# Kernel tuning notes

Hardware: AMD Instinct MI355X
Metric: run time of the kernel (lower is better)

## Reference

```python
import jax, jax.numpy as jnp
import numpy as np
import math

D_MODEL, N_HEADS, D_FF = 1024, 16, 4096
B, S = 2, 2048
EPS = 1e-8
NEG = -1e9


def setup_inputs() -> dict:
    key = jax.random.key(0)
    ks = jax.random.split(key, 8)
    sc = 0.02
    return {
        "x": jax.random.normal(ks[0], (B, S, D_MODEL), dtype=jnp.float32),
        "mask": jnp.ones((B, 1, 1, S), dtype=jnp.int32),
        "Wq": jax.random.normal(ks[1], (D_MODEL, D_MODEL), dtype=jnp.float32) * sc,
        "bq": jnp.zeros((D_MODEL,), dtype=jnp.float32),
        "Wk": jax.random.normal(ks[2], (D_MODEL, D_MODEL), dtype=jnp.float32) * sc,
        "bk": jnp.zeros((D_MODEL,), dtype=jnp.float32),
        "Wv": jax.random.normal(ks[3], (D_MODEL, D_MODEL), dtype=jnp.float32) * sc,
        "bv": jnp.zeros((D_MODEL,), dtype=jnp.float32),
        "Wo": jax.random.normal(ks[4], (D_MODEL, D_MODEL), dtype=jnp.float32) * sc,
        "bo": jnp.zeros((D_MODEL,), dtype=jnp.float32),
        "W1": jax.random.normal(ks[5], (D_FF, D_MODEL), dtype=jnp.float32) * sc,
        "b1": jnp.zeros((D_FF,), dtype=jnp.float32),
        "W2": jax.random.normal(ks[6], (D_MODEL, D_FF), dtype=jnp.float32) * sc,
        "b2": jnp.zeros((D_MODEL,), dtype=jnp.float32),
        "g1": jnp.ones((1, 1, 1), dtype=jnp.float32),
        "be1": jnp.zeros((1, 1, 1), dtype=jnp.float32),
        "g2": jnp.ones((1, 1, 1), dtype=jnp.float32),
        "be2": jnp.zeros((1, 1, 1), dtype=jnp.float32),
    }


def _layernorm(x, gamma, beta):
    # Matches torch: mean / unbiased std (ddof=1), eps added to std (not var)
    mean = jnp.mean(x, axis=-1, keepdims=True)
    std = jnp.std(x, axis=-1, keepdims=True, ddof=1)
    return gamma * (x - mean) / (std + EPS) + beta


def reference(x, mask, Wq, bq, Wk, bk, Wv, bv, Wo, bo, W1, b1, W2, b2, g1, be1, g2, be2):
    dk = D_MODEL // N_HEADS

    # --- pre-norm self-attention + residual ---
    h = _layernorm(x, g1, be1)
    q = h @ Wq.T + bq
    k = h @ Wk.T + bk
    v = h @ Wv.T + bv
    # [B,S,D] -> [B,H,S,dk]
    q = q.reshape(B, S, N_HEADS, dk).transpose(0, 2, 1, 3)
    k = k.reshape(B, S, N_HEADS, dk).transpose(0, 2, 1, 3)
    v = v.reshape(B, S, N_HEADS, dk).transpose(0, 2, 1, 3)
    scores = jnp.einsum('bhqd,bhkd->bhqk', q, k) / math.sqrt(dk)
    scores = jnp.where(mask == 0, NEG, scores)
    attn = jax.nn.softmax(scores, axis=-1)
    ctx = jnp.einsum('bhqk,bhkd->bhqd', attn, v)  # [B,H,S,dk]
    ctx = ctx.transpose(0, 2, 1, 3).reshape(B, S, D_MODEL)
    x = x + (ctx @ Wo.T + bo)

    # --- pre-norm FFN + residual ---
    h2 = _layernorm(x, g2, be2)
    f = jax.nn.relu(h2 @ W1.T + b1) @ W2.T + b2
    return x + f
```

## Files before the change

kernel.cpp:

```cpp
#include <hip/hip_runtime.h>
#include <math.h>

#define D_MODEL 1024
#define N_HEADS 16
#define DK      64
#define D_FF    4096
#define BB      2
#define SS      2048
#define ROWS    (BB * SS)
#define EPS     1e-8f
#define NEG     -1e9f
#define QSCALE  0.1803368801111f
#define DEFER_THR 11.541560327f

union F4 { float4 v; float f[4]; };

typedef __attribute__((ext_vector_type(8))) short   bf16x8;
typedef __attribute__((ext_vector_type(4))) float   f32x4;

__device__ __forceinline__ unsigned short f2bf(float f) {
    union { float f; unsigned u; } a; a.f = f;
    unsigned r = a.u + 0x7FFFu + ((a.u >> 16) & 1u);
    return (unsigned short)(r >> 16);
}

__device__ __forceinline__ float exp2_fast(float x) {
    float r;
    asm("v_exp_f32 %0, %1" : "=v"(r) : "v"(x));
    return r;
}

__device__ __forceinline__ unsigned cvt_pk_bf16(float lo, float hi) {
    unsigned r;
    asm("v_cvt_pk_bf16_f32 %0, %1, %2" : "=v"(r) : "v"(lo), "v"(hi));
    return r;
}

__device__ __forceinline__ void gload16(const void* g, void* l) {
    __builtin_amdgcn_global_load_lds(
        (const __attribute__((address_space(1))) unsigned int*)g,
        (__attribute__((address_space(3))) unsigned int*)l, 16, 0, 0);
}

__global__ __launch_bounds__(256) void ln_bf16_kernel(const float* __restrict__ x,
                                                      const float* __restrict__ g,
                                                      const float* __restrict__ be,
                                                      unsigned short* __restrict__ out) {
    __shared__ float sm[8];
    const int row = blockIdx.x;
    float4 v = ((const float4*)(x + (size_t)row * D_MODEL))[threadIdx.x];

    float s = v.x + v.y + v.z + v.w;
#pragma unroll
    for (int o = 32; o; o >>= 1) s += __shfl_xor(s, o);
    const int wid = threadIdx.x >> 6, lane = threadIdx.x & 63;
    if (lane == 0) sm[wid] = s;
    __syncthreads();
    const float mean = (sm[0] + sm[1] + sm[2] + sm[3]) * (1.0f / D_MODEL);

    const float dx = v.x - mean, dy = v.y - mean, dz = v.z - mean, dw = v.w - mean;
    float sq = dx * dx + dy * dy + dz * dz + dw * dw;
#pragma unroll
    for (int o = 32; o; o >>= 1) sq += __shfl_xor(sq, o);
    if (lane == 0) sm[4 + wid] = sq;
    __syncthreads();
    const float var = (sm[4] + sm[5] + sm[6] + sm[7]) * (1.0f / (D_MODEL - 1));
    const float inv = 1.0f / (sqrtf(var) + EPS);
    const float g0 = g[0], b0 = be[0];

    ushort4 o4;
    o4.x = f2bf(g0 * dx * inv + b0);
    o4.y = f2bf(g0 * dy * inv + b0);
    o4.z = f2bf(g0 * dz * inv + b0);
    o4.w = f2bf(g0 * dw * inv + b0);
    ((ushort4*)(out + (size_t)row * D_MODEL))[threadIdx.x] = o4;
}

__global__ __launch_bounds__(256) void cast_all(const float* __restrict__ s0,
                                                const float* __restrict__ s1,
                                                const float* __restrict__ s2,
                                                const float* __restrict__ s3,
                                                const float* __restrict__ s4,
                                                const float* __restrict__ s5,
                                                unsigned short* __restrict__ d0,
                                                unsigned short* __restrict__ d1,
                                                unsigned short* __restrict__ d2,
                                                unsigned short* __restrict__ d3,
                                                unsigned short* __restrict__ d4,
                                                unsigned short* __restrict__ d5) {
    const int ND4 = D_MODEL * D_MODEL / 4;
    const int NF4 = D_FF * D_MODEL / 4;
    const int total = 4 * ND4 + 2 * NF4;
    for (int i = blockIdx.x * 256 + threadIdx.x; i < total; i += gridDim.x * 256) {
        const float* s; unsigned short* d; int off;
        if (i < 4 * ND4) {
            const int w = i >> 18;
            off = i & (ND4 - 1);
            s = (w == 0) ? s0 : (w == 1) ? s1 : (w == 2) ? s2 : s3;
            d = (w == 0) ? d0 : (w == 1) ? d1 : (w == 2) ? d2 : d3;
        } else {
            const int j = i - 4 * ND4;
            const int w = j >> 20;
            off = j & (NF4 - 1);
            s = w ? s5 : s4;
            d = w ? d5 : d4;
        }
        float4 v = ((const float4*)s)[off];
        ushort4 o = { f2bf(v.x), f2bf(v.y), f2bf(v.z), f2bf(v.w) };
        ((ushort4*)d)[off] = o;
    }
}

__global__ __launch_bounds__(256) void mask_prep(const int* __restrict__ mask,
                                                 float* __restrict__ mbias,
                                                 int* __restrict__ tflag) {
    const int i = blockIdx.x * 256 + threadIdx.x;
    const int m = mask[i];
    mbias[i] = m ? 0.0f : NEG;
    unsigned long long z = __ballot(m == 0);
    if ((threadIdx.x & 63) == 0) tflag[i >> 6] = (z != 0ull) ? 1 : 0;
}

template <bool RELU, bool RES, bool OUTBF, bool BROW>
__device__ __forceinline__ void gemm_core(const unsigned short* __restrict__ A,
                                          const unsigned short* __restrict__ B,
                                          const float* __restrict__ bias,
                                          const float* __restrict__ res,
                                          void* __restrict__ Cout,
                                          int M, int N, int K, float scale,
                                          int bm, int bn,
                                          unsigned short* As, unsigned short* Bs) {
    const int tid  = threadIdx.x;
    const int lane = tid & 63;
    const int wv   = tid >> 6;
    const int wr   = wv >> 1, wc = wv & 1;
    const int lr   = lane & 15, lq = lane >> 4;

    f32x4 acc[4][4];
#pragma unroll
    for (int m = 0; m < 4; ++m)
#pragma unroll
        for (int n = 0; n < 4; ++n)
            acc[m][n] = (f32x4){0.f, 0.f, 0.f, 0.f};

    const int srow = wv * 32 + (lane >> 2);
    const int scol = (lane & 3) * 8;

    auto stage = [&](int buf, int k0) {
        unsigned short* ab = As + buf * 4096;
        unsigned short* bb = Bs + buf * 4096;
        gload16(A + (size_t)(bm + srow) * K + k0 + scol,      &ab[(wv * 32) * 32]);
        gload16(A + (size_t)(bm + srow + 16) * K + k0 + scol, &ab[(wv * 32 + 16) * 32]);
        gload16(B + (size_t)(bn + srow) * K + k0 + scol,      &bb[(wv * 32) * 32]);
        gload16(B + (size_t)(bn + srow + 16) * K + k0 + scol, &bb[(wv * 32 + 16) * 32]);
    };

    const int T = K >> 5;
    stage(0, 0);
    __syncthreads();

    for (int t = 0; t < T; ++t) {
        const int cur = t & 1;
        if (t + 1 < T) stage(cur ^ 1, (t + 1) << 5);
        __builtin_amdgcn_sched_barrier(0);

        const unsigned short* ab = As + cur * 4096;
        const unsigned short* bb = Bs + cur * 4096;
        bf16x8 af[4], bf[4];
#pragma unroll
        for (int m = 0; m < 4; ++m)
            af[m] = *(const bf16x8*)&ab[(wr * 64 + m * 16 + lr) * 32 + lq * 8];
#pragma unroll
        for (int n = 0; n < 4; ++n)
            bf[n] = *(const bf16x8*)&bb[(wc * 64 + n * 16 + lr) * 32 + lq * 8];

#pragma unroll
        for (int m = 0; m < 4; ++m)
#pragma unroll
            for (int n = 0; n < 4; ++n)
                acc[m][n] = __builtin_amdgcn_mfma_f32_16x16x32_bf16(af[m], bf[n], acc[m][n], 0, 0, 0);

        __syncthreads();
    }

#pragma unroll
    for (int n = 0; n < 4; ++n) {
        const int col = bn + wc * 64 + n * 16 + lr;
        const float bcol = BROW ? 0.0f : bias[col];
#pragma unroll
        for (int m = 0; m < 4; ++m) {
#pragma unroll
            for (int r = 0; r < 4; ++r) {
                const int row = bm + wr * 64 + m * 16 + lq * 4 + r;
                float v = acc[m][n][r] + (BROW ? bias[row] : bcol);
                v *= scale;
                if (RELU) v = fmaxf(v, 0.0f);
                if (RES)  v += res[(size_t)row * N + col];
                if (OUTBF) ((unsigned short*)Cout)[(size_t)row * N + col] = f2bf(v);
                else       ((float*)Cout)[(size_t)row * N + col] = v;
            }
        }
    }
}

template <bool RELU, bool RES, bool OUTBF, bool BROW>
__global__ __launch_bounds__(256) void gemm_bf16(const unsigned short* __restrict__ A,
                                                 const unsigned short* __restrict__ B,
                                                 const float* __restrict__ bias,
                                                 const float* __restrict__ res,
                                                 void* __restrict__ Cout,
                                                 int M, int N, int K, float scale) {
    __shared__ unsigned short As[2 * 4096];
    __shared__ unsigned short Bs[2 * 4096];
    gemm_core<RELU, RES, OUTBF, BROW>(A, B, bias, res, Cout, M, N, K, scale,
                                      blockIdx.y * 128, blockIdx.x * 128, As, Bs);
}

template <bool RELU, bool RES, bool OUTBF>
__global__ __launch_bounds__(256) void gemm_n64(const unsigned short* __restrict__ A,
                                                const unsigned short* __restrict__ B,
                                                const float* __restrict__ bias,
                                                const float* __restrict__ res,
                                                void* __restrict__ Cout,
                                                int M, int N, int K, float scale) {
    __shared__ unsigned short As[2 * 4096];
    __shared__ unsigned short Bs[2 * 2048];

    const int bm = blockIdx.y * 128;
    const int bn = blockIdx.x * 64;
    const int tid  = threadIdx.x;
    const int lane = tid & 63;
    const int wv   = tid >> 6;
    const int wr   = wv >> 1, wc = wv & 1;
    const int lr   = lane & 15, lq = lane >> 4;

    f32x4 acc[4][2];
#pragma unroll
    for (int m = 0; m < 4; ++m)
#pragma unroll
        for (int n = 0; n < 2; ++n)
            acc[m][n] = (f32x4){0.f, 0.f, 0.f, 0.f};

    const int sra = wv * 32 + (lane >> 2);
    const int srb = wv * 16 + (lane >> 2);
    const int scol = (lane & 3) * 8;

    auto stage = [&](int buf, int k0) {
        unsigned short* ab = As + buf * 4096;
        unsigned short* bb = Bs + buf * 2048;
        gload16(A + (size_t)(bm + sra) * K + k0 + scol,      &ab[(wv * 32) * 32]);
        gload16(A + (size_t)(bm + sra + 16) * K + k0 + scol, &ab[(wv * 32 + 16) * 32]);
        gload16(B + (size_t)(bn + srb) * K + k0 + scol,      &bb[(wv * 16) * 32]);
    };

    const int T = K >> 5;
    stage(0, 0);
    __syncthreads();

    for (int t = 0; t < T; ++t) {
        const int cur = t & 1;
        if (t + 1 < T) stage(cur ^ 1, (t + 1) << 5);
        __builtin_amdgcn_sched_barrier(0);

        const unsigned short* ab = As + cur * 4096;
        const unsigned short* bb = Bs + cur * 2048;
        bf16x8 af[4], bf[2];
#pragma unroll
        for (int m = 0; m < 4; ++m)
            af[m] = *(const bf16x8*)&ab[(wr * 64 + m * 16 + lr) * 32 + lq * 8];
#pragma unroll
        for (int n = 0; n < 2; ++n)
            bf[n] = *(const bf16x8*)&bb[(wc * 32 + n * 16 + lr) * 32 + lq * 8];

#pragma unroll
        for (int m = 0; m < 4; ++m)
#pragma unroll
            for (int n = 0; n < 2; ++n)
                acc[m][n] = __builtin_amdgcn_mfma_f32_16x16x32_bf16(af[m], bf[n], acc[m][n], 0, 0, 0);

        __syncthreads();
    }

#pragma unroll
    for (int n = 0; n < 2; ++n) {
        const int col = bn + wc * 32 + n * 16 + lr;
        const float bcol = bias[col];
#pragma unroll
        for (int m = 0; m < 4; ++m) {
#pragma unroll
            for (int r = 0; r < 4; ++r) {
                const int row = bm + wr * 64 + m * 16 + lq * 4 + r;
                float v = acc[m][n][r] + bcol;
                v *= scale;
                if (RELU) v = fmaxf(v, 0.0f);
                if (RES)  v += res[(size_t)row * N + col];
                if (OUTBF) ((unsigned short*)Cout)[(size_t)row * N + col] = f2bf(v);
                else       ((float*)Cout)[(size_t)row * N + col] = v;
            }
        }
    }
}

__global__ __launch_bounds__(256) void qkv_fused(const unsigned short* __restrict__ h,
                                                 const unsigned short* __restrict__ Wq,
                                                 const unsigned short* __restrict__ Wk,
                                                 const unsigned short* __restrict__ Wv,
                                                 const float* __restrict__ bq,
                                                 const float* __restrict__ bk,
                                                 const float* __restrict__ bv,
                                                 unsigned short* __restrict__ qo,
                                                 unsigned short* __restrict__ ko,
                                                 unsigned short* __restrict__ vto) {
    __shared__ unsigned short As[2 * 4096];
    __shared__ unsigned short Bs[2 * 4096];
    const int id = blockIdx.x;
    const int op = id >> 8;
    const int t  = id & 255;
    if (op == 0) {
        gemm_core<false, false, true, false>(h, Wq, bq, nullptr, qo,
            ROWS, D_MODEL, D_MODEL, QSCALE, (t >> 3) * 128, (t & 7) * 128, As, Bs);
    } else if (op == 1) {
        gemm_core<false, false, true, false>(h, Wk, bk, nullptr, ko,
            ROWS, D_MODEL, D_MODEL, 1.0f, (t >> 3) * 128, (t & 7) * 128, As, Bs);
    } else {
        gemm_core<false, false, true, true>(Wv, h, bv, nullptr, vto,
            D_MODEL, ROWS, D_MODEL, 1.0f, (t >> 5) * 128, (t & 31) * 128, As, Bs);
    }
}

__global__ __launch_bounds__(256) void attn_mfma(const unsigned short* __restrict__ Q,
                                                 const unsigned short* __restrict__ K,
                                                 const unsigned short* __restrict__ Vt,
                                                 const float* __restrict__ mbias,
                                                 const int* __restrict__ tflag,
                                                 unsigned short* __restrict__ O) {
    __shared__ unsigned short Ks[2][64][68];
    __shared__ unsigned short Vs[2][64][68];
    __shared__ unsigned short Ps[64][68];

    const int bh = blockIdx.x, qt = blockIdx.y;
    const int b = bh >> 4, h = bh & 15;
    const int q0 = qt * 64;
    const int tid = threadIdx.x;
    const int w = tid >> 6, lane = tid & 63;
    const int lr = lane & 15, lq = lane >> 4;

    const size_t qkbase = (size_t)b * SS * D_MODEL + (size_t)h * DK;
    const int tok0 = b * SS;
    const float* mb = mbias + (size_t)b * SS;
    const int* tf = tflag + b * (SS / 64);

    const unsigned short* qp = Q + qkbase + (size_t)(q0 + w * 16 + lr) * D_MODEL;
    const bf16x8 qf0 = *(const bf16x8*)(qp + lq * 8);
    const bf16x8 qf1 = *(const bf16x8*)(qp + 32 + lq * 8);

    const int sr = tid >> 3, sch = tid & 7;
    bf16x8 kreg0, kreg1, vreg0, vreg1;
    {
        const unsigned short* kp = K + qkbase + (size_t)sr * D_MODEL + sch * 8;
        kreg0 = *(const bf16x8*)(kp);
        kreg1 = *(const bf16x8*)(kp + 32 * D_MODEL);
        const unsigned short* vp = Vt + (size_t)(h * DK + sr) * ROWS + tok0 + sch * 8;
        vreg0 = *(const bf16x8*)(vp);
        vreg1 = *(const bf16x8*)(vp + 32 * ROWS);
    }
    *(bf16x8*)&Ks[0][sr][sch * 8]      = kreg0;
    *(bf16x8*)&Ks[0][sr + 32][sch * 8] = kreg1;
    *(bf16x8*)&Vs[0][sr][sch * 8]      = vreg0;
    *(bf16x8*)&Vs[0][sr + 32][sch * 8] = vreg1;
    __syncthreads();

    f32x4 acc_o[4];
#pragma unroll
    for (int n = 0; n < 4; ++n) acc_o[n] = (f32x4){0.f, 0.f, 0.f, 0.f};
    float m_run = -1e30f, l_run = 0.0f;

    const int NT = SS / 64;
    for (int kt = 0; kt < NT; ++kt) {
        const int cur = kt & 1;
        if (kt + 1 < NT) {
            const int k1 = (kt + 1) * 64;
            const unsigned short* kp = K + qkbase + (size_t)(k1 + sr) * D_MODEL + sch * 8;
            kreg0 = *(const bf16x8*)(kp);
            kreg1 = *(const bf16x8*)(kp + 32 * D_MODEL);
            const unsigned short* vp = Vt + (size_t)(h * DK + sr) * ROWS + tok0 + k1 + sch * 8;
            vreg0 = *(const bf16x8*)(vp);
            vreg1 = *(const bf16x8*)(vp + 32 * ROWS);
        }

        f32x4 sa[4];
#pragma unroll
        for (int n = 0; n < 4; ++n) sa[n] = (f32x4){0.f, 0.f, 0.f, 0.f};
        __builtin_amdgcn_s_setprio(1);
#pragma unroll
        for (int n = 0; n < 4; ++n) {
            bf16x8 kf0 = *(const bf16x8*)&Ks[cur][n * 16 + lr][lq * 8];
            bf16x8 kf1 = *(const bf16x8*)&Ks[cur][n * 16 + lr][32 + lq * 8];
            sa[n] = __builtin_amdgcn_mfma_f32_16x16x32_bf16(kf0, qf0, sa[n], 0, 0, 0);
            sa[n] = __builtin_amdgcn_mfma_f32_16x16x32_bf16(kf1, qf1, sa[n], 0, 0, 0);
        }
        __builtin_amdgcn_s_setprio(0);

        if (tf[kt]) {
#pragma unroll
            for (int n = 0; n < 4; ++n) {
                F4 m4; m4.v = *(const float4*)&mb[kt * 64 + n * 16 + lq * 4];
#pragma unroll
                for (int r = 0; r < 4; ++r) sa[n][r] += m4.f[r];
            }
        }

        float pmax = sa[0][0];
#pragma unroll
        for (int n = 0; n < 4; ++n)
#pragma unroll
            for (int r = 0; r < 4; ++r) pmax = fmaxf(pmax, sa[n][r]);
        pmax = fmaxf(pmax, __shfl_xor(pmax, 16));
        pmax = fmaxf(pmax, __shfl_xor(pmax, 32));

        if (!__all(pmax - m_run <= DEFER_THR)) {
            const float mn = fmaxf(m_run, pmax);
            const float sc = exp2_fast(m_run - mn);
            m_run = mn;
            l_run *= sc;
#pragma unroll
            for (int n = 0; n < 4; ++n) {
                acc_o[n][0] *= sc; acc_o[n][1] *= sc; acc_o[n][2] *= sc; acc_o[n][3] *= sc;
            }
        }
        float rs = 0.0f;
#pragma unroll
        for (int n = 0; n < 4; ++n)
#pragma unroll
            for (int r = 0; r < 4; ++r) {
                const float p = exp2_fast(sa[n][r] - m_run);
                sa[n][r] = p;
                rs += p;
            }
        rs += __shfl_xor(rs, 16);
        rs += __shfl_xor(rs, 32);
        l_run += rs;

#pragma unroll
        for (int n = 0; n < 4; ++n) {
            uint2 u;
            u.x = cvt_pk_bf16(sa[n][0], sa[n][1]);
            u.y = cvt_pk_bf16(sa[n][2], sa[n][3]);
            *(uint2*)&Ps[w * 16 + lr][n * 16 + lq * 4] = u;
        }

        __builtin_amdgcn_s_setprio(1);
#pragma unroll
        for (int c = 0; c < 2; ++c) {
            bf16x8 pf = *(const bf16x8*)&Ps[w * 16 + lr][c * 32 + lq * 8];
#pragma unroll
            for (int n = 0; n < 4; ++n) {
                bf16x8 vf = *(const bf16x8*)&Vs[cur][n * 16 + lr][c * 32 + lq * 8];
                acc_o[n] = __builtin_amdgcn_mfma_f32_16x16x32_bf16(vf, pf, acc_o[n], 0, 0, 0);
            }
        }
        __builtin_amdgcn_s_setprio(0);

        if (kt + 1 < NT) {
            *(bf16x8*)&Ks[cur ^ 1][sr][sch * 8]      = kreg0;
            *(bf16x8*)&Ks[cur ^ 1][sr + 32][sch * 8] = kreg1;
            *(bf16x8*)&Vs[cur ^ 1][sr][sch * 8]      = vreg0;
            *(bf16x8*)&Vs[cur ^ 1][sr + 32][sch * 8] = vreg1;
        }
        __syncthreads();
    }

    const float invl = 1.0f / l_run;
    unsigned short* orow = O + qkbase + (size_t)(q0 + w * 16 + lr) * D_MODEL;
#pragma unroll
    for (int n = 0; n < 4; ++n) {
        ushort4 o;
        o.x = f2bf(acc_o[n][0] * invl);
        o.y = f2bf(acc_o[n][1] * invl);
        o.z = f2bf(acc_o[n][2] * invl);
        o.w = f2bf(acc_o[n][3] * invl);
        *(ushort4*)(orow + n * 16 + lq * 4) = o;
    }
}

extern "C" void kernel_launch(void* const* d_in, const int* in_sizes, int n_in,
                              void* d_out, int out_size, void* d_ws, size_t ws_size,
                              hipStream_t stream) {
    const float* x   = (const float*)d_in[0];
    const int*   msk = (const int*)d_in[1];
    const float* Wq  = (const float*)d_in[2];
    const float* bq  = (const float*)d_in[3];
    const float* Wk  = (const float*)d_in[4];
    const float* bk  = (const float*)d_in[5];
    const float* Wv  = (const float*)d_in[6];
    const float* bv  = (const float*)d_in[7];
    const float* Wo  = (const float*)d_in[8];
    const float* bo  = (const float*)d_in[9];
    const float* W1  = (const float*)d_in[10];
    const float* b1  = (const float*)d_in[11];
    const float* W2  = (const float*)d_in[12];
    const float* b2  = (const float*)d_in[13];
    const float* g1  = (const float*)d_in[14];
    const float* be1 = (const float*)d_in[15];
    const float* g2  = (const float*)d_in[16];
    const float* be2 = (const float*)d_in[17];
    float* out = (float*)d_out;

    char* w = (char*)d_ws;
    unsigned short* h_bf   = (unsigned short*)w; w += (size_t)ROWS * D_MODEL * 2;
    unsigned short* qb_bf  = (unsigned short*)w; w += (size_t)ROWS * D_MODEL * 2;
    unsigned short* kb_bf  = (unsigned short*)w; w += (size_t)ROWS * D_MODEL * 2;
    unsigned short* vt_bf  = (unsigned short*)w; w += (size_t)ROWS * D_MODEL * 2;
    unsigned short* ctx_bf = (unsigned short*)w; w += (size_t)ROWS * D_MODEL * 2;
    float* xat             = (float*)w;          w += (size_t)ROWS * D_MODEL * 4;
    unsigned short* h2_bf  = (unsigned short*)w; w += (size_t)ROWS * D_MODEL * 2;
    unsigned short* ff1_bf = (unsigned short*)w; w += (size_t)ROWS * D_FF * 2;
    unsigned short* Wq_bf  = (unsigned short*)w; w += (size_t)D_MODEL * D_MODEL * 2;
    unsigned short* Wk_bf  = (unsigned short*)w; w += (size_t)D_MODEL * D_MODEL * 2;
    unsigned short* Wv_bf  = (unsigned short*)w; w += (size_t)D_MODEL * D_MODEL * 2;
    unsigned short* Wo_bf  = (unsigned short*)w; w += (size_t)D_MODEL * D_MODEL * 2;
    unsigned short* W1_bf  = (unsigned short*)w; w += (size_t)D_FF * D_MODEL * 2;
    unsigned short* W2_bf  = (unsigned short*)w; w += (size_t)D_FF * D_MODEL * 2;
    float* mbias           = (float*)w;          w += (size_t)ROWS * 4;
    int* tflag             = (int*)w;            w += (size_t)(BB * SS / 64) * 4;

    const dim3 blk(256);
    cast_all<<<2048, blk, 0, stream>>>(Wq, Wk, Wv, Wo, W1, W2,
                                       Wq_bf, Wk_bf, Wv_bf, Wo_bf, W1_bf, W2_bf);
    mask_prep<<<ROWS / 256, blk, 0, stream>>>(msk, mbias, tflag);

    ln_bf16_kernel<<<ROWS, blk, 0, stream>>>(x, g1, be1, h_bf);

    qkv_fused<<<768, blk, 0, stream>>>(h_bf, Wq_bf, Wk_bf, Wv_bf, bq, bk, bv,
                                       qb_bf, kb_bf, vt_bf);

    attn_mfma<<<dim3(BB * N_HEADS, SS / 64), blk, 0, stream>>>(qb_bf, kb_bf, vt_bf,
                                                               mbias, tflag, ctx_bf);

    gemm_n64<false, true, false><<<dim3(D_MODEL / 64, ROWS / 128), blk, 0, stream>>>(
        ctx_bf, Wo_bf, bo, x, xat, ROWS, D_MODEL, D_MODEL, 1.0f);

    ln_bf16_kernel<<<ROWS, blk, 0, stream>>>(xat, g2, be2, h2_bf);

    gemm_bf16<true, false, true, false><<<dim3(D_FF / 128, ROWS / 128), blk, 0, stream>>>(
        h2_bf, W1_bf, b1, nullptr, ff1_bf, ROWS, D_FF, D_MODEL, 1.0f);

    gemm_n64<false, true, false><<<dim3(D_MODEL / 64, ROWS / 128), blk, 0, stream>>>(
        ff1_bf, W2_bf, b2, xat, out, ROWS, D_MODEL, D_FF, 1.0f);
}
```

Measured before the change: 405.8 us.

## Split-K the FFN2 GEMM, fold mask prep into cast, single-buffer attention K/V

The FFN down-projection now runs as a two-way split-K GEMM with 128x128 tiles. Each half writes fp32 partials into reused workspace, and a separate combine kernel adds bias and residual. Mask preparation is merged into the weight-cast kernel to save one launch. The attention kernel drops its K/V LDS double buffer and the s_setprio hints in favour of a single buffer with two barriers per tile, which cuts LDS use but may expose load latency.

```diff
diff --git a/kernel.cpp b/kernel.cpp
--- a/kernel.cpp
+++ b/kernel.cpp
@@ -87,11 +87,20 @@
                                                 unsigned short* __restrict__ d2,
                                                 unsigned short* __restrict__ d3,
                                                 unsigned short* __restrict__ d4,
-                                                unsigned short* __restrict__ d5) {
+                                                unsigned short* __restrict__ d5,
+                                                const int* __restrict__ mask,
+                                                float* __restrict__ mbias,
+                                                int* __restrict__ tflag) {
     const int ND4 = D_MODEL * D_MODEL / 4;
     const int NF4 = D_FF * D_MODEL / 4;
     const int total = 4 * ND4 + 2 * NF4;
     for (int i = blockIdx.x * 256 + threadIdx.x; i < total; i += gridDim.x * 256) {
+        if (i < ROWS) {
+            const int m = mask[i];
+            mbias[i] = m ? 0.0f : NEG;
+            unsigned long long z = __ballot(m == 0);
+            if ((threadIdx.x & 63) == 0) tflag[i >> 6] = (z != 0ull) ? 1 : 0;
+        }
         const float* s; unsigned short* d; int off;
         if (i < 4 * ND4) {
             const int w = i >> 18;
@@ -109,16 +118,6 @@
         ushort4 o = { f2bf(v.x), f2bf(v.y), f2bf(v.z), f2bf(v.w) };
         ((ushort4*)d)[off] = o;
     }
-}
-
-__global__ __launch_bounds__(256) void mask_prep(const int* __restrict__ mask,
-                                                 float* __restrict__ mbias,
-                                                 int* __restrict__ tflag) {
-    const int i = blockIdx.x * 256 + threadIdx.x;
-    const int m = mask[i];
-    mbias[i] = m ? 0.0f : NEG;
-    unsigned long long z = __ballot(m == 0);
-    if ((threadIdx.x & 63) == 0) tflag[i >> 6] = (z != 0ull) ? 1 : 0;
 }
 
 template <bool RELU, bool RES, bool OUTBF, bool BROW>
@@ -214,6 +213,103 @@
     __shared__ unsigned short Bs[2 * 4096];
     gemm_core<RELU, RES, OUTBF, BROW>(A, B, bias, res, Cout, M, N, K, scale,
                                       blockIdx.y * 128, blockIdx.x * 128, As, Bs);
+}
+
+__global__ __launch_bounds__(256) void gemm_splitk(const unsigned short* __restrict__ A,
+                                                   const unsigned short* __restrict__ B,
+                                                   float* __restrict__ Cpart,
+                                                   int M, int N, int K, int klen) {
+    __shared__ unsigned short As[2 * 4096];
+    __shared__ unsigned short Bs[2 * 4096];
+
+    const int bm = blockIdx.y * 128;
+    const int bn = blockIdx.x * 128;
+    const int kb0 = blockIdx.z * klen;
+    float* Cz = Cpart + (size_t)blockIdx.z * M * N;
+
+    const int tid  = threadIdx.x;
+    const int lane = tid & 63;
+    const int wv   = tid >> 6;
+    const int wr   = wv >> 1, wc = wv & 1;
+    const int lr   = lane & 15, lq = lane >> 4;
+
+    f32x4 acc[4][4];
+#pragma unroll
+    for (int m = 0; m < 4; ++m)
+#pragma unroll
+        for (int n = 0; n < 4; ++n)
+            acc[m][n] = (f32x4){0.f, 0.f, 0.f, 0.f};
+
+    const int srow = wv * 32 + (lane >> 2);
+    const int scol = (lane & 3) * 8;
+
+    auto stage = [&](int buf, int k0) {
+        unsigned short* ab = As + buf * 4096;
+        unsigned short* bb = Bs + buf * 4096;
+        gload16(A + (size_t)(bm + srow) * K + k0 + scol,      &ab[(wv * 32) * 32]);
+        gload16(A + (size_t)(bm + srow + 16) * K + k0 + scol, &ab[(wv * 32 + 16) * 32]);
+        gload16(B + (size_t)(bn + srow) * K + k0 + scol,      &bb[(wv * 32) * 32]);
+        gload16(B + (size_t)(bn + srow + 16) * K + k0 + scol, &bb[(wv * 32 + 16) * 32]);
+    };
+
+    const int T = klen >> 5;
+    stage(0, kb0);
+    __syncthreads();
+
+    for (int t = 0; t < T; ++t) {
+        const int cur = t & 1;
+        if (t + 1 < T) stage(cur ^ 1, kb0 + ((t + 1) << 5));
+        __builtin_amdgcn_sched_barrier(0);
+
+        const unsigned short* ab = As + cur * 4096;
+        const unsigned short* bb = Bs + cur * 4096;
+        bf16x8 af[4], bf[4];
+#pragma unroll
+        for (int m = 0; m < 4; ++m)
+            af[m] = *(const bf16x8*)&ab[(wr * 64 + m * 16 + lr) * 32 + lq * 8];
+#pragma unroll
+        for (int n = 0; n < 4; ++n)
+            bf[n] = *(const bf16x8*)&bb[(wc * 64 + n * 16 + lr) * 32 + lq * 8];
+
+#pragma unroll
+        for (int m = 0; m < 4; ++m)
+#pragma unroll
+            for (int n = 0; n < 4; ++n)
+                acc[m][n] = __builtin_amdgcn_mfma_f32_16x16x32_bf16(af[m], bf[n], acc[m][n], 0, 0, 0);
+
+        __syncthreads();
+    }
+
+#pragma unroll
+    for (int n = 0; n < 4; ++n) {
+        const int col = bn + wc * 64 + n * 16 + lr;
+#pragma unroll
+        for (int m = 0; m < 4; ++m)
+#pragma unroll
+            for (int r = 0; r < 4; ++r) {
+                const int row = bm + wr * 64 + m * 16 + lq * 4 + r;
+                Cz[(size_t)row * N + col] = acc[m][n][r];
+            }
+    }
+}
+
+__global__ __launch_bounds__(256) void ffn2_combine(const float* __restrict__ p0,
+                                                    const float* __restrict__ p1,
+                                                    const float* __restrict__ bias,
+                                                    const float* __restrict__ res,
+                                                    float* __restrict__ out) {
+    const int i = blockIdx.x * 256 + threadIdx.x;
+    const int c4 = i & (D_MODEL / 4 - 1);
+    float4 a = ((const float4*)p0)[i];
+    float4 b = ((const float4*)p1)[i];
+    float4 r = ((const float4*)res)[i];
+    float4 bb = ((const float4*)bias)[c4];
+    float4 o;
+    o.x = a.x + b.x + bb.x + r.x;
+    o.y = a.y + b.y + bb.y + r.y;
+    o.z = a.z + b.z + bb.z + r.z;
+    o.w = a.w + b.w + bb.w + r.w;
+    ((float4*)out)[i] = o;
 }
 
 template <bool RELU, bool RES, bool OUTBF>
@@ -334,8 +430,8 @@
                                                  const float* __restrict__ mbias,
                                                  const int* __restrict__ tflag,
                                                  unsigned short* __restrict__ O) {
-    __shared__ unsigned short Ks[2][64][68];
-    __shared__ unsigned short Vs[2][64][68];
+    __shared__ unsigned short Ks[64][68];
+    __shared__ unsigned short Vs[64][68];
     __shared__ unsigned short Ps[64][68];
 
     const int bh = blockIdx.x, qt = blockIdx.y;
@@ -364,11 +460,6 @@
         vreg0 = *(const bf16x8*)(vp);
         vreg1 = *(const bf16x8*)(vp + 32 * ROWS);
     }
-    *(bf16x8*)&Ks[0][sr][sch * 8]      = kreg0;
-    *(bf16x8*)&Ks[0][sr + 32][sch * 8] = kreg1;
-    *(bf16x8*)&Vs[0][sr][sch * 8]      = vreg0;
-    *(bf16x8*)&Vs[0][sr + 32][sch * 8] = vreg1;
-    __syncthreads();
 
     f32x4 acc_o[4];
 #pragma unroll
@@ -377,7 +468,13 @@
 
     const int NT = SS / 64;
     for (int kt = 0; kt < NT; ++kt) {
-        const int cur = kt & 1;
+        __syncthreads();
+        *(bf16x8*)&Ks[sr][sch * 8]      = kreg0;
+        *(bf16x8*)&Ks[sr + 32][sch * 8] = kreg1;
+        *(bf16x8*)&Vs[sr][sch * 8]      = vreg0;
+        *(bf16x8*)&Vs[sr + 32][sch * 8] = vreg1;
+        __syncthreads();
+
         if (kt + 1 < NT) {
             const int k1 = (kt + 1) * 64;
             const unsigned short* kp = K + qkbase + (size_t)(k1 + sr) * D_MODEL + sch * 8;
@@ -391,15 +488,13 @@
         f32x4 sa[4];
 #pragma unroll
         for (int n = 0; n < 4; ++n) sa[n] = (f32x4){0.f, 0.f, 0.f, 0.f};
-        __builtin_amdgcn_s_setprio(1);
 #pragma unroll
         for (int n = 0; n < 4; ++n) {
-            bf16x8 kf0 = *(const bf16x8*)&Ks[cur][n * 16 + lr][lq * 8];
-            bf16x8 kf1 = *(const bf16x8*)&Ks[cur][n * 16 + lr][32 + lq * 8];
+            bf16x8 kf0 = *(const bf16x8*)&Ks[n * 16 + lr][lq * 8];
+            bf16x8 kf1 = *(const bf16x8*)&Ks[n * 16 + lr][32 + lq * 8];
             sa[n] = __builtin_amdgcn_mfma_f32_16x16x32_bf16(kf0, qf0, sa[n], 0, 0, 0);
             sa[n] = __builtin_amdgcn_mfma_f32_16x16x32_bf16(kf1, qf1, sa[n], 0, 0, 0);
         }
-        __builtin_amdgcn_s_setprio(0);
 
         if (tf[kt]) {
 #pragma unroll
@@ -449,25 +544,15 @@
             *(uint2*)&Ps[w * 16 + lr][n * 16 + lq * 4] = u;
         }
 
-        __builtin_amdgcn_s_setprio(1);
 #pragma unroll
         for (int c = 0; c < 2; ++c) {
             bf16x8 pf = *(const bf16x8*)&Ps[w * 16 + lr][c * 32 + lq * 8];
 #pragma unroll
             for (int n = 0; n < 4; ++n) {
-                bf16x8 vf = *(const bf16x8*)&Vs[cur][n * 16 + lr][c * 32 + lq * 8];
+                bf16x8 vf = *(const bf16x8*)&Vs[n * 16 + lr][c * 32 + lq * 8];
                 acc_o[n] = __builtin_amdgcn_mfma_f32_16x16x32_bf16(vf, pf, acc_o[n], 0, 0, 0);
             }
         }
-        __builtin_amdgcn_s_setprio(0);
-
-        if (kt + 1 < NT) {
-            *(bf16x8*)&Ks[cur ^ 1][sr][sch * 8]      = kreg0;
-            *(bf16x8*)&Ks[cur ^ 1][sr + 32][sch * 8] = kreg1;
-            *(bf16x8*)&Vs[cur ^ 1][sr][sch * 8]      = vreg0;
-            *(bf16x8*)&Vs[cur ^ 1][sr + 32][sch * 8] = vreg1;
-        }
-        __syncthreads();
     }
 
     const float invl = 1.0f / l_run;
@@ -524,10 +609,12 @@
     float* mbias           = (float*)w;          w += (size_t)ROWS * 4;
     int* tflag             = (int*)w;            w += (size_t)(BB * SS / 64) * 4;
 
+    float* part = (float*)qb_bf;
+
     const dim3 blk(256);
     cast_all<<<2048, blk, 0, stream>>>(Wq, Wk, Wv, Wo, W1, W2,
-                                       Wq_bf, Wk_bf, Wv_bf, Wo_bf, W1_bf, W2_bf);
-    mask_prep<<<ROWS / 256, blk, 0, stream>>>(msk, mbias, tflag);
+                                       Wq_bf, Wk_bf, Wv_bf, Wo_bf, W1_bf, W2_bf,
+                                       msk, mbias, tflag);
 
     ln_bf16_kernel<<<ROWS, blk, 0, stream>>>(x, g1, be1, h_bf);
 
@@ -545,6 +632,8 @@
     gemm_bf16<true, false, true, false><<<dim3(D_FF / 128, ROWS / 128), blk, 0, stream>>>(
         h2_bf, W1_bf, b1, nullptr, ff1_bf, ROWS, D_FF, D_MODEL, 1.0f);
 
-    gemm_n64<false, true, false><<<dim3(D_MODEL / 64, ROWS / 128), blk, 0, stream>>>(
-        ff1_bf, W2_bf, b2, xat, out, ROWS, D_MODEL, D_FF, 1.0f);
-}
+    gemm_splitk<<<dim3(D_MODEL / 128, ROWS / 128, 2), blk, 0, stream>>>(
+        ff1_bf, W2_bf, part, ROWS, D_MODEL, D_FF, D_FF / 2);
+    ffn2_combine<<<ROWS * D_MODEL / 4 / 256, blk, 0, stream>>>(
+        part, part + (size_t)ROWS * D_MODEL, b2, xat, out);
+}
```

Result: faster. 386.1 us (-4.9%).
